# Performance work log

Measured on AMD Instinct MI355X. Metric: run time of the kernel, lower is better.

The kernel has to match this reference:

```python
import jax, jax.numpy as jnp
import numpy as np
from jax import lax

N_CLASS = 21
K_ED = 5
ALPHA = 0.1
BN_EPS = 1e-5


def _conv(x, w):
    # NCHW conv, stride 1, SAME padding
    return lax.conv_general_dilated(x, w, (1, 1), 'SAME',
                                    dimension_numbers=('NCHW', 'OIHW', 'NCHW'))


def _bn(x, g, b, m, v):
    # inference-mode BatchNorm2d with running stats
    scale = (g * lax.rsqrt(v + BN_EPS))[None, :, None, None]
    return (x - m[None, :, None, None]) * scale + b[None, :, None, None]


def _maxpool(x, k):
    return lax.reduce_window(x, -jnp.inf, lax.max, (1, 1, k, k), (1, 1, 1, 1), 'SAME')


def setup_inputs() -> dict:
    key = jax.random.key(0)
    ks = jax.random.split(key, 12)
    N, F, H, W, C = 8, 512, 96, 96, N_CLASS
    feature = jax.random.normal(ks[0], (N, F, H, W), jnp.float32)
    global_pred = jax.random.normal(ks[1], (N, C, H, W), jnp.float32)
    conv1_w = jax.random.normal(ks[2], (256, F, 3, 3), jnp.float32) * 0.02
    bn1_g = jnp.ones((256,), jnp.float32)
    bn1_b = jnp.zeros((256,), jnp.float32)
    bn1_m = jax.random.normal(ks[3], (256,), jnp.float32) * 0.1
    bn1_v = jax.random.uniform(ks[4], (256,), jnp.float32, 0.5, 1.5)
    conv2_w = jax.random.normal(ks[5], (128, 256, 3, 3), jnp.float32) * 0.02
    bn2_g = jnp.ones((128,), jnp.float32)
    bn2_b = jnp.zeros((128,), jnp.float32)
    bn2_m = jax.random.normal(ks[6], (128,), jnp.float32) * 0.1
    bn2_v = jax.random.uniform(ks[7], (128,), jnp.float32, 0.5, 1.5)
    conv3_w = jax.random.normal(ks[8], (C, 128, 1, 1), jnp.float32) * 0.02
    conv3_b = jnp.zeros((C,), jnp.float32)
    return dict(feature=feature, global_pred=global_pred,
                conv1_w=conv1_w, bn1_g=bn1_g, bn1_b=bn1_b, bn1_m=bn1_m, bn1_v=bn1_v,
                conv2_w=conv2_w, bn2_g=bn2_g, bn2_b=bn2_b, bn2_m=bn2_m, bn2_v=bn2_v,
                conv3_w=conv3_w, conv3_b=conv3_b)


def reference(feature, global_pred, conv1_w, bn1_g, bn1_b, bn1_m, bn1_v,
              conv2_w, bn2_g, bn2_b, bn2_m, bn2_v, conv3_w, conv3_b):
    N, F, H, W = feature.shape
    # hard labels -> one-hot [N, C, H, W]
    lbl = jnp.argmax(global_pred, axis=1)
    onehot = jnp.transpose(jax.nn.one_hot(lbl, N_CLASS, dtype=feature.dtype), (0, 3, 1, 2))
    # binary morphology: dilation = max-pool, erosion = -max-pool(-x)
    d = _maxpool(onehot, K_ED)
    e = -_maxpool(-onehot, K_ED)
    transition = jnp.sum(d - e, axis=1, keepdims=True)
    transition = jnp.where(transition >= 1.0, 1.0, transition)  # [N,1,H,W]
    tfeat = feature * transition
    # per-class masked mean over ALL H*W pixels (faithful to .mean(dim=2))
    objs = jnp.einsum('nfhw,nchw->ncf', feature, e) / (H * W)  # [N,C,F]
    # cdist(p=2) between transition-feature pixels and class prototypes
    x = tfeat.reshape(N, F, H * W).transpose(0, 2, 1)  # [N,HW,F]
    x2 = jnp.sum(x * x, axis=-1, keepdims=True)
    o2 = jnp.sum(objs * objs, axis=-1)
    d2 = jnp.maximum(x2 + o2[:, None, :] - 2.0 * jnp.einsum('npf,ncf->npc', x, objs), 0.0)
    cd = jnp.where(d2 > 0, jnp.sqrt(jnp.where(d2 > 0, d2, 1.0)), 0.0)  # safe sqrt
    dist = 1.0 - jax.nn.softmax(cd, axis=-1)  # [N,HW,C]
    obj_feat = jnp.einsum('npc,ncf->nfp', dist, objs).reshape(N, F, H, W)
    fusion = (feature * (1.0 - transition)
              + feature * transition * ALPHA
              + obj_feat * transition * (1.0 - ALPHA))
    # fusion_predictor: convBNReLU -> bilinear x2 -> convBNReLU -> 1x1 conv
    h = jax.nn.relu(_bn(_conv(fusion, conv1_w), bn1_g, bn1_b, bn1_m, bn1_v))
    h = jax.image.resize(h, (N, 256, 2 * H, 2 * W), method='bilinear')
    h = jax.nn.relu(_bn(_conv(h, conv2_w), bn2_g, bn2_b, bn2_m, bn2_v))
    logits = _conv(h, conv3_w) + conv3_b[None, :, None, None]
    # eval mode: softmax over classes
    return jax.nn.softmax(logits, axis=1)
```

## Files before the change

### kernel.cpp

```cpp
#include <hip/hip_runtime.h>
#include <cstdint>
#include <cstddef>

typedef __attribute__((ext_vector_type(4))) float f32x4;
typedef __attribute__((ext_vector_type(8))) short short8;

__device__ __forceinline__ float bf2f(unsigned short u) {
  union { unsigned int i; float f; } x; x.i = ((unsigned int)u) << 16; return x.f;
}
__device__ __forceinline__ unsigned short f2bf(float f) {
  union { float f; unsigned int i; } x; x.f = f;
  unsigned int r = x.i + 0x7fffu + ((x.i >> 16) & 1u);
  return (unsigned short)(r >> 16);
}
__device__ __forceinline__ void gload16(unsigned short* lds, const unsigned short* g) {
  __builtin_amdgcn_global_load_lds(
      (const __attribute__((address_space(1))) unsigned int*)g,
      (__attribute__((address_space(3))) unsigned int*)lds, 16, 0, 0);
}

__global__ void k_prep(const float* __restrict__ w1, const float* __restrict__ w2,
                       const float* __restrict__ w3,
                       const float* __restrict__ g1, const float* __restrict__ b1,
                       const float* __restrict__ m1, const float* __restrict__ v1,
                       const float* __restrict__ g2, const float* __restrict__ b2,
                       const float* __restrict__ m2, const float* __restrict__ v2,
                       unsigned short* __restrict__ w1t, unsigned short* __restrict__ w2t,
                       unsigned short* __restrict__ w3b,
                       float* __restrict__ s1, float* __restrict__ bb1,
                       float* __restrict__ s2, float* __restrict__ bb2) {
  const int blk = blockIdx.x;
  const int tid = threadIdx.x;
  if (blk < 4608) {
    int i = blk * 256 + tid;
    int o = i / 4608, k = i - o * 4608;
    int cblk = k / 288, r = k - cblk * 288;
    int t = r >> 5, cl = r & 31;
    int ci = cblk * 32 + cl;
    int ty = t / 3, tx = t - ty * 3;
    w1t[i] = f2bf(w1[((o * 512 + ci) * 3 + ty) * 3 + tx]);
  } else if (blk < 5760) {
    int i = (blk - 4608) * 256 + tid;
    int o = i / 2304, k = i - o * 2304;
    int cblk = k / 288, r = k - cblk * 288;
    int t = r >> 5, cl = r & 31;
    int ci = cblk * 32 + cl;
    int ty = t / 3, tx = t - ty * 3;
    w2t[i] = f2bf(w2[((o * 256 + ci) * 3 + ty) * 3 + tx]);
  } else if (blk < 5776) {
    int i = (blk - 5760) * 256 + tid;
    int c = i >> 7, k = i & 127;
    w3b[i] = (c < 21) ? f2bf(w3[c * 128 + k]) : (unsigned short)0;
  } else {
    if (tid < 256) { float s = g1[tid] * rsqrtf(v1[tid] + 1e-5f); s1[tid] = s; bb1[tid] = b1[tid] - m1[tid] * s; }
    if (tid < 128) { float s = g2[tid] * rsqrtf(v2[tid] + 1e-5f); s2[tid] = s; bb2[tid] = b2[tid] - m2[tid] * s; }
  }
}

__global__ void k_labels_init(const float* __restrict__ gp, signed char* __restrict__ lab,
                              unsigned short* __restrict__ fuP, float* __restrict__ objs) {
  const int blk = blockIdx.x;
  const int tid = threadIdx.x;
  if (blk < 288) {
    int p = blk * 256 + tid;
    int n = p / 9216, q = p - n * 9216;
    const float* g = gp + (long)n * 21 * 9216 + q;
    float best = g[0]; int bi = 0;
    #pragma unroll
    for (int c = 1; c < 21; c++) {
      float v = g[(long)c * 9216];
      if (v > best) { best = v; bi = c; }
    }
    lab[p] = (signed char)bi;
  } else if (blk < 1064) {
    int i = (blk - 288) * 256 + tid;
    const int B = 2 * 98 + 2 * 96;
    const int cg = i & 63; int b = i >> 6;
    const int n = b / B; b -= n * B;
    int y, x;
    if (b < 98) { y = 0; x = b; }
    else if (b < 196) { y = 97; x = b - 98; }
    else { int r = b - 196; y = 1 + (r >> 1); x = (r & 1) ? 97 : 0; }
    short8 z = {0, 0, 0, 0, 0, 0, 0, 0};
    *(short8*)&fuP[(((long)n * 98 + y) * 98 + x) * 512 + cg * 8] = z;
  } else {
    int i = (blk - 1064) * 256 + tid;
    objs[i] = 0.f;
  }
}

__global__ void k_em(const signed char* __restrict__ lab, signed char* __restrict__ em) {
  int p = blockIdx.x * 256 + threadIdx.x;
  int n = p / 9216, q = p - n * 9216, y = q / 96, x = q - y * 96;
  const signed char* L = lab + n * 9216;
  signed char l0 = L[q];
  bool uni = true;
  for (int dy = -2; dy <= 2; dy++) {
    int yy = y + dy; if (yy < 0 || yy > 95) continue;
    for (int dx = -2; dx <= 2; dx++) {
      int xx = x + dx; if (xx < 0 || xx > 95) continue;
      uni = uni && (L[yy * 96 + xx] == l0);
    }
  }
  em[p] = uni ? l0 : (signed char)-1;
}

__global__ __launch_bounds__(256)
void k_featT_objs(const float* __restrict__ feat, const signed char* __restrict__ em,
                  unsigned short* __restrict__ featT, float* __restrict__ objs) {
  __shared__ float part[21 * 128];
  __shared__ int pres[21];
  const int g = blockIdx.x * 256 + threadIdx.x;
  const int n = g / 9216, p = g - n * 9216;
  const int fg0 = blockIdx.y * 16;
  const int tid = threadIdx.x;
  for (int i = tid; i < 21 * 128; i += 256) part[i] = 0.f;
  if (tid < 21) pres[tid] = 0;
  __syncthreads();
  const int c0 = em[g];
  if (c0 >= 0) pres[c0] = 1;
  const float* src = feat + (long)n * 512 * 9216 + p;
  unsigned short* dst = featT + ((long)n * 9216 + p) * 512;
  for (int fg = fg0; fg < fg0 + 16; fg++) {
    short8 o;
    float fv[8];
    #pragma unroll
    for (int j = 0; j < 8; j++) {
      fv[j] = src[(long)(fg * 8 + j) * 9216];
      o[j] = (short)f2bf(fv[j]);
    }
    *(short8*)&dst[fg * 8] = o;
    if (c0 >= 0) {
      const int lf0 = (fg - fg0) * 8;
      #pragma unroll
      for (int j = 0; j < 8; j++) atomicAdd(&part[c0 * 128 + lf0 + j], fv[j]);
    }
  }
  __syncthreads();
  for (int i = tid; i < 21 * 128; i += 256) {
    const int c = i >> 7, lf = i & 127;
    if (pres[c])
      atomicAdd(&objs[((long)n * 21 + c) * 512 + blockIdx.y * 128 + lf],
                part[i] * (1.0f / 9216.0f));
  }
}

__global__ void k_objfin(const float* __restrict__ objs, float* __restrict__ o2,
                         unsigned short* __restrict__ oc) {
  const int b = blockIdx.x;
  const int n = b >> 5, c = b & 31;
  const int lane = threadIdx.x;
  unsigned short* dst = oc + ((long)n * 32 + c) * 512;
  if (c < 21) {
    const float* o = objs + ((long)n * 21 + c) * 512;
    float s = 0.f;
    for (int f = lane; f < 512; f += 64) {
      float v = o[f];
      s += v * v;
      dst[f] = f2bf(v);
    }
    #pragma unroll
    for (int off = 32; off; off >>= 1) s += __shfl_down(s, off);
    if (lane == 0) o2[n * 21 + c] = s;
  } else {
    for (int f = lane; f < 512; f += 64) dst[f] = 0;
  }
}

__global__ __launch_bounds__(256)
void k_dist_fusion(const unsigned short* __restrict__ featT,
                   const unsigned short* __restrict__ objs_c,
                   const float* __restrict__ o2, const float* __restrict__ objs,
                   const signed char* __restrict__ em,
                   unsigned short* __restrict__ fuP) {
  __shared__ float ob[21 * 512];
  __shared__ float dl[64][21];
  __shared__ signed char eml[64];
  const int n = blockIdx.y;
  const int p0 = blockIdx.x * 64;
  const int tid = threadIdx.x;
  const int w = tid >> 6, lane = tid & 63;
  const int lrow = lane & 15, kg = lane >> 4;

  for (int i = tid; i < 21 * 512; i += 256) ob[i] = objs[(long)n * 21 * 512 + i];
  if (tid < 64) eml[tid] = em[n * 9216 + p0 + tid];

  const int px = p0 + w * 16 + lrow;
  const unsigned short* fb = featT + ((long)n * 9216 + px) * 512 + kg * 8;
  const unsigned short* a0p = objs_c + ((long)n * 32 + lrow) * 512 + kg * 8;
  const unsigned short* a1p = a0p + 16 * 512;
  f32x4 acc0 = {0.f, 0.f, 0.f, 0.f}, acc1 = {0.f, 0.f, 0.f, 0.f};
  float x2 = 0.f;
  #pragma unroll
  for (int s = 0; s < 16; s++) {
    const short8 b = *(const short8*)&fb[s * 32];
    const short8 a0 = *(const short8*)&a0p[s * 32];
    const short8 a1 = *(const short8*)&a1p[s * 32];
    acc0 = __builtin_amdgcn_mfma_f32_16x16x32_bf16(a0, b, acc0, 0, 0, 0);
    acc1 = __builtin_amdgcn_mfma_f32_16x16x32_bf16(a1, b, acc1, 0, 0, 0);
    #pragma unroll
    for (int j = 0; j < 8; j++) { float v = bf2f((unsigned short)b[j]); x2 += v * v; }
  }
  x2 += __shfl_xor(x2, 16); x2 += __shfl_xor(x2, 32);
  float cd[8], mx = -1e30f;
  #pragma unroll
  for (int r = 0; r < 4; r++) {
    const int c = kg * 4 + r;
    float d2 = x2 + o2[n * 21 + c] - 2.f * acc0[r];
    cd[r] = sqrtf(fmaxf(d2, 0.f)); mx = fmaxf(mx, cd[r]);
  }
  #pragma unroll
  for (int r = 0; r < 4; r++) {
    const int c = 16 + kg * 4 + r;
    if (c < 21) {
      float d2 = x2 + o2[n * 21 + c] - 2.f * acc1[r];
      cd[4 + r] = sqrtf(fmaxf(d2, 0.f)); mx = fmaxf(mx, cd[4 + r]);
    } else cd[4 + r] = -1e30f;
  }
  mx = fmaxf(mx, __shfl_xor(mx, 16)); mx = fmaxf(mx, __shfl_xor(mx, 32));
  float sum = 0.f;
  #pragma unroll
  for (int k = 0; k < 8; k++) {
    cd[k] = (cd[k] > -1e29f) ? __expf(cd[k] - mx) : 0.f;
    sum += cd[k];
  }
  sum += __shfl_xor(sum, 16); sum += __shfl_xor(sum, 32);
  const float inv = 1.f / sum;
  const int lpx = w * 16 + lrow;
  #pragma unroll
  for (int r = 0; r < 4; r++) dl[lpx][kg * 4 + r] = 1.f - cd[r] * inv;
  #pragma unroll
  for (int r = 0; r < 4; r++) {
    const int c = 16 + kg * 4 + r;
    if (c < 21) dl[lpx][c] = 1.f - cd[4 + r] * inv;
  }
  __syncthreads();

  const int px2 = tid & 63;
  const int fg = (tid >> 6) * 8;
  const int q = p0 + px2;
  const int y = q / 96, x = q - y * 96;
  unsigned short* dst = fuP + (((long)n * 98 + y + 1) * 98 + (x + 1)) * 512;
  const bool t = eml[px2] < 0;
  const unsigned short* srcT = featT + ((long)n * 9216 + q) * 512;
  for (int f0 = 0; f0 < 512; f0 += 32) {
    short8 o;
    const short8 fvv = *(const short8*)&srcT[f0 + fg];
    #pragma unroll
    for (int j = 0; j < 8; j++) {
      const int f = f0 + fg + j;
      float fv = bf2f((unsigned short)fvv[j]);
      if (t) {
        float of = 0.f;
        #pragma unroll
        for (int c = 0; c < 21; c++) of += dl[px2][c] * ob[c * 512 + f];
        fv = 0.1f * fv + 0.9f * of;
      }
      o[j] = (short)f2bf(fv);
    }
    *(short8*)&dst[fg] = o;
    dst += 32;
  }
}

template <int CIN, int NK>
__global__ __launch_bounds__(256)
void conv3x3_gemm(const unsigned short* __restrict__ inP,
                  const unsigned short* __restrict__ wT,
                  const float* __restrict__ scale, const float* __restrict__ bias,
                  unsigned short* __restrict__ out,
                  int Hout, int Wout, int Hp, int Wp, int COUT, int nbN) {
  __shared__ unsigned short ldsA[3][4096];
  __shared__ unsigned short ldsB[3][4096];
  const int tid = threadIdx.x;
  const int chunk = gridDim.x >> 3;
  const int bid = (blockIdx.x & 7) * chunk + (blockIdx.x >> 3);
  const int mb = bid / nbN, nb = bid - mb * nbN;
  const int bm0 = mb * 128, bn0 = nb * 128;
  const int KT = 9 * CIN;
  const int HWo = Hout * Wout;

  const int rA = tid >> 2;
  const int ch8 = (((tid & 3) ^ ((tid >> 3) & 3)) * 8);
  const int m0 = bm0 + rA, m1 = m0 + 64;
  const int n0 = m0 / HWo; const int q0 = m0 - n0 * HWo;
  const int y0 = q0 / Wout, x0 = q0 - y0 * Wout;
  const int n1 = m1 / HWo; const int q1 = m1 - n1 * HWo;
  const int y1 = q1 / Wout, x1 = q1 - y1 * Wout;
  const unsigned short* gA0 = inP + ((long)(n0 * Hp + y0) * Wp + x0) * CIN + ch8;
  const unsigned short* gA1 = inP + ((long)(n1 * Hp + y1) * Wp + x1) * CIN + ch8;
  const unsigned short* gB0 = wT + (long)(bn0 + rA) * KT + ch8;
  const unsigned short* gB1 = wT + (long)(bn0 + rA + 64) * KT + ch8;

  const int lane = tid & 63;
  const int wv = tid >> 6;
  const int wr = wv >> 1, wc = wv & 1;
  const int lrow = lane & 15, kg = lane >> 4;
  const int arow = wr * 64 + lrow;
  const int aoff = arow * 32 + (kg ^ ((arow >> 1) & 3)) * 8;
  const int brow = wc * 64 + lrow;
  const int boff = brow * 32 + (kg ^ ((brow >> 1) & 3)) * 8;

  f32x4 acc[4][4];
  const f32x4 zero = {0.f, 0.f, 0.f, 0.f};
  #pragma unroll
  for (int i = 0; i < 4; i++)
    #pragma unroll
    for (int j = 0; j < 4; j++) acc[i][j] = zero;

  auto stage = [&](int b, int s) {
    const int cblk = s / 9;
    const int t = s - cblk * 9;
    const int ty = t / 3, tx = t - ty * 3;
    const long offA = (long)(ty * Wp + tx) * CIN + cblk * 32;
    gload16(&ldsA[b][tid * 8], gA0 + offA);
    gload16(&ldsA[b][2048 + tid * 8], gA1 + offA);
    const long k0 = (long)s * 32;
    gload16(&ldsB[b][tid * 8], gB0 + k0);
    gload16(&ldsB[b][2048 + tid * 8], gB1 + k0);
  };

  auto kstep = [&](int rd) {
    const unsigned short* A = ldsA[rd];
    const unsigned short* B = ldsB[rd];
    short8 af[4], bfr[4];
    #pragma unroll
    for (int i = 0; i < 4; i++) af[i] = *(const short8*)&A[aoff + i * 512];
    #pragma unroll
    for (int j = 0; j < 4; j++) bfr[j] = *(const short8*)&B[boff + j * 512];
    __builtin_amdgcn_s_setprio(1);
    #pragma unroll
    for (int i = 0; i < 4; i++)
      #pragma unroll
      for (int j = 0; j < 4; j++)
        acc[i][j] = __builtin_amdgcn_mfma_f32_16x16x32_bf16(af[i], bfr[j], acc[i][j], 0, 0, 0);
    __builtin_amdgcn_s_setprio(0);
  };

  stage(0, 0);
  stage(1, 1);
  int rd = 0, prev = 2;
  for (int s = 0; s < NK - 2; ++s) {
    __builtin_amdgcn_s_barrier();
    asm volatile("" ::: "memory");
    stage(prev, s + 2);
    asm volatile("s_waitcnt vmcnt(8)" ::: "memory");
    __builtin_amdgcn_s_barrier();
    asm volatile("" ::: "memory");
    kstep(rd);
    prev = rd; rd = (rd == 2) ? 0 : rd + 1;
  }
  asm volatile("s_waitcnt vmcnt(4)" ::: "memory");
  __builtin_amdgcn_s_barrier();
  asm volatile("" ::: "memory");
  kstep(rd);
  rd = (rd == 2) ? 0 : rd + 1;
  asm volatile("s_waitcnt vmcnt(0)" ::: "memory");
  __builtin_amdgcn_s_barrier();
  asm volatile("" ::: "memory");
  kstep(rd);

  #pragma unroll
  for (int i = 0; i < 4; i++) {
    const int row = bm0 + wr * 64 + i * 16 + kg * 4;
    #pragma unroll
    for (int j = 0; j < 4; j++) {
      const int col = bn0 + wc * 64 + j * 16 + lrow;
      const float sc = scale[col], bi = bias[col];
      #pragma unroll
      for (int r = 0; r < 4; r++) {
        float v = acc[i][j][r] * sc + bi;
        v = v > 0.f ? v : 0.f;
        out[(long)(row + r) * COUT + col] = f2bf(v);
      }
    }
  }
}

__global__ __launch_bounds__(256)
void conv2_fused(const unsigned short* __restrict__ inP,
                 const unsigned short* __restrict__ wT,
                 const float* __restrict__ scale, const float* __restrict__ bias,
                 const unsigned short* __restrict__ w3b, const float* __restrict__ b3,
                 float* __restrict__ out) {
  constexpr int CIN = 256, NK = 72;
  constexpr int Wout = 192, Hp = 194, Wp = 194;
  constexpr int HWo = 192 * 192;
  constexpr int KT = 9 * CIN;
  __shared__ unsigned short pool[6 * 4096];
  const int tid = threadIdx.x;
  const int chunk = gridDim.x >> 3;
  const int bid = (blockIdx.x & 7) * chunk + (blockIdx.x >> 3);
  const int bm0 = bid * 128;

  const int rA = tid >> 2;
  const int ch8 = (((tid & 3) ^ ((tid >> 3) & 3)) * 8);
  const int m0 = bm0 + rA, m1 = m0 + 64;
  const int n0 = m0 / HWo; const int q0 = m0 - n0 * HWo;
  const int y0 = q0 / Wout, x0 = q0 - y0 * Wout;
  const int n1 = m1 / HWo; const int q1 = m1 - n1 * HWo;
  const int y1 = q1 / Wout, x1 = q1 - y1 * Wout;
  const unsigned short* gA0 = inP + ((long)(n0 * Hp + y0) * Wp + x0) * CIN + ch8;
  const unsigned short* gA1 = inP + ((long)(n1 * Hp + y1) * Wp + x1) * CIN + ch8;
  const unsigned short* gB0 = wT + (long)rA * KT + ch8;
  const unsigned short* gB1 = wT + (long)(rA + 64) * KT + ch8;

  const int lane = tid & 63;
  const int wv = tid >> 6;
  const int wr = wv >> 1, wc = wv & 1;
  const int lrow = lane & 15, kg = lane >> 4;
  const int arow = wr * 64 + lrow;
  const int aoff = arow * 32 + (kg ^ ((arow >> 1) & 3)) * 8;
  const int brow = wc * 64 + lrow;
  const int boff = brow * 32 + (kg ^ ((brow >> 1) & 3)) * 8;

  f32x4 acc[4][4];
  const f32x4 zero = {0.f, 0.f, 0.f, 0.f};
  #pragma unroll
  for (int i = 0; i < 4; i++)
    #pragma unroll
    for (int j = 0; j < 4; j++) acc[i][j] = zero;

  auto stage = [&](int b, int s) {
    const int cblk = s / 9;
    const int t = s - cblk * 9;
    const int ty = t / 3, tx = t - ty * 3;
    const long offA = (long)(ty * Wp + tx) * CIN + cblk * 32;
    gload16(&pool[b * 4096 + tid * 8], gA0 + offA);
    gload16(&pool[b * 4096 + 2048 + tid * 8], gA1 + offA);
    const long k0 = (long)s * 32;
    gload16(&pool[12288 + b * 4096 + tid * 8], gB0 + k0);
    gload16(&pool[12288 + b * 4096 + 2048 + tid * 8], gB1 + k0);
  };

  auto kstep = [&](int rd) {
    const unsigned short* A = &pool[rd * 4096];
    const unsigned short* B = &pool[12288 + rd * 4096];
    short8 af[4], bfr[4];
    #pragma unroll
    for (int i = 0; i < 4; i++) af[i] = *(const short8*)&A[aoff + i * 512];
    #pragma unroll
    for (int j = 0; j < 4; j++) bfr[j] = *(const short8*)&B[boff + j * 512];
    __builtin_amdgcn_s_setprio(1);
    #pragma unroll
    for (int i = 0; i < 4; i++)
      #pragma unroll
      for (int j = 0; j < 4; j++)
        acc[i][j] = __builtin_amdgcn_mfma_f32_16x16x32_bf16(af[i], bfr[j], acc[i][j], 0, 0, 0);
    __builtin_amdgcn_s_setprio(0);
  };

  stage(0, 0);
  stage(1, 1);
  int rd = 0;
  for (int s = 0; s < NK; ++s) {
    if (s < NK - 1)
      asm volatile("s_waitcnt vmcnt(4)" ::: "memory");
    else
      asm volatile("s_waitcnt vmcnt(0)" ::: "memory");
    __builtin_amdgcn_s_barrier();
    asm volatile("" ::: "memory");
    kstep(rd);
    if (s + 2 < NK) stage((rd + 2 >= 3) ? rd - 1 : rd + 2, s + 2);
    rd = (rd == 2) ? 0 : rd + 1;
  }

  asm volatile("s_waitcnt lgkmcnt(0)" ::: "memory");
  __builtin_amdgcn_s_barrier();
  asm volatile("" ::: "memory");
  #pragma unroll
  for (int j = 0; j < 4; j++) {
    const int ch = wc * 64 + j * 16 + lrow;
    const float sc = scale[ch], bi = bias[ch];
    #pragma unroll
    for (int i = 0; i < 4; i++) {
      const int pxb = wr * 64 + i * 16 + kg * 4;
      #pragma unroll
      for (int r = 0; r < 4; r++) {
        const int px = pxb + r;
        float v = acc[i][j][r] * sc + bi;
        v = v > 0.f ? v : 0.f;
        pool[px * 128 + (ch ^ ((px & 7) << 3))] = f2bf(v);
      }
    }
  }
  asm volatile("s_waitcnt lgkmcnt(0)" ::: "memory");
  __builtin_amdgcn_s_barrier();
  asm volatile("" ::: "memory");

  #pragma unroll
  for (int g = 0; g < 2; g++) {
    const int px = wv * 32 + g * 16 + lrow;
    f32x4 acc0 = {0.f, 0.f, 0.f, 0.f}, acc1 = {0.f, 0.f, 0.f, 0.f};
    #pragma unroll
    for (int s = 0; s < 4; s++) {
      const int ch0 = s * 32 + kg * 8;
      const short8 b = *(const short8*)&pool[px * 128 + (ch0 ^ ((px & 7) << 3))];
      const short8 a0 = *(const short8*)&w3b[lrow * 128 + ch0];
      const short8 a1 = *(const short8*)&w3b[(16 + lrow) * 128 + ch0];
      acc0 = __builtin_amdgcn_mfma_f32_16x16x32_bf16(a0, b, acc0, 0, 0, 0);
      acc1 = __builtin_amdgcn_mfma_f32_16x16x32_bf16(a1, b, acc1, 0, 0, 0);
    }
    float lg[8], mx = -1e30f;
    #pragma unroll
    for (int r = 0; r < 4; r++) {
      lg[r] = acc0[r] + b3[kg * 4 + r];
      mx = fmaxf(mx, lg[r]);
    }
    #pragma unroll
    for (int r = 0; r < 4; r++) {
      const int c = 16 + kg * 4 + r;
      if (c < 21) { lg[4 + r] = acc1[r] + b3[c]; mx = fmaxf(mx, lg[4 + r]); }
      else lg[4 + r] = -1e30f;
    }
    mx = fmaxf(mx, __shfl_xor(mx, 16)); mx = fmaxf(mx, __shfl_xor(mx, 32));
    float sum = 0.f;
    #pragma unroll
    for (int k = 0; k < 8; k++) {
      lg[k] = (lg[k] > -1e29f) ? __expf(lg[k] - mx) : 0.f;
      sum += lg[k];
    }
    sum += __shfl_xor(sum, 16); sum += __shfl_xor(sum, 32);
    const float inv = 1.f / sum;
    const int m = bm0 + px;
    const int n = m / HWo;
    const int q = m - n * HWo;
    #pragma unroll
    for (int r = 0; r < 4; r++)
      out[((long)n * 21 + kg * 4 + r) * (long)HWo + q] = lg[r] * inv;
    #pragma unroll
    for (int r = 0; r < 4; r++) {
      const int c = 16 + kg * 4 + r;
      if (c < 21) out[((long)n * 21 + c) * (long)HWo + q] = lg[4 + r] * inv;
    }
  }
}

__global__ void k_upsample(const unsigned short* __restrict__ h1,
                           unsigned short* __restrict__ h2P) {
  if (blockIdx.x >= 36864) {
    int i = (blockIdx.x - 36864) * 256 + threadIdx.x;
    const int B = 2 * 194 + 2 * 192;
    const int cg = i & 31; int b = i >> 5;
    const int n = b / B; b -= n * B;
    int y, x;
    if (b < 194) { y = 0; x = b; }
    else if (b < 388) { y = 193; x = b - 194; }
    else { int r = b - 388; y = 1 + (r >> 1); x = (r & 1) ? 193 : 0; }
    short8 z = {0, 0, 0, 0, 0, 0, 0, 0};
    *(short8*)&h2P[(((long)n * 194 + y) * 194 + x) * 256 + cg * 8] = z;
    return;
  }
  const int idx = blockIdx.x * 256 + threadIdx.x;
  const int c8 = (idx & 31) * 8;
  const int p = idx >> 5;
  const int n = p / 36864; const int rr = p - n * 36864;
  const int Y = rr / 192, X = rr - Y * 192;
  const int ky = Y >> 1, kx = X >> 1;
  int yA, yB, xA, xB; float wyA, wyB, wxA, wxB;
  if ((Y & 1) == 0) { yA = ky > 0 ? ky - 1 : 0; yB = ky; wyA = 0.25f; wyB = 0.75f; }
  else { yA = ky; yB = ky < 95 ? ky + 1 : 95; wyA = 0.75f; wyB = 0.25f; }
  if ((X & 1) == 0) { xA = kx > 0 ? kx - 1 : 0; xB = kx; wxA = 0.25f; wxB = 0.75f; }
  else { xA = kx; xB = kx < 95 ? kx + 1 : 95; wxA = 0.75f; wxB = 0.25f; }
  const unsigned short* hb = h1 + (long)n * 96 * 96 * 256 + c8;
  const short8 vaa = *(const short8*)&hb[((long)yA * 96 + xA) * 256];
  const short8 vab = *(const short8*)&hb[((long)yA * 96 + xB) * 256];
  const short8 vba = *(const short8*)&hb[((long)yB * 96 + xA) * 256];
  const short8 vbb = *(const short8*)&hb[((long)yB * 96 + xB) * 256];
  short8 o;
  #pragma unroll
  for (int j = 0; j < 8; j++) {
    float v = wyA * (wxA * bf2f((unsigned short)vaa[j]) + wxB * bf2f((unsigned short)vab[j])) +
              wyB * (wxA * bf2f((unsigned short)vba[j]) + wxB * bf2f((unsigned short)vbb[j]));
    o[j] = (short)f2bf(v);
  }
  *(short8*)&h2P[(((long)n * 194 + Y + 1) * 194 + X + 1) * 256 + c8] = o;
}

extern "C" void kernel_launch(void* const* d_in, const int* in_sizes, int n_in,
                              void* d_out, int out_size, void* d_ws, size_t ws_size,
                              hipStream_t stream) {
  const float* feature = (const float*)d_in[0];
  const float* gp = (const float*)d_in[1];
  const float* w1 = (const float*)d_in[2];
  const float* g1 = (const float*)d_in[3];
  const float* b1 = (const float*)d_in[4];
  const float* m1 = (const float*)d_in[5];
  const float* v1 = (const float*)d_in[6];
  const float* w2 = (const float*)d_in[7];
  const float* g2 = (const float*)d_in[8];
  const float* b2 = (const float*)d_in[9];
  const float* m2 = (const float*)d_in[10];
  const float* v2 = (const float*)d_in[11];
  const float* w3 = (const float*)d_in[12];
  const float* b3 = (const float*)d_in[13];
  float* out = (float*)d_out;

  char* ws = (char*)d_ws;
  size_t off = 0;
  auto alloc = [&](size_t bytes) -> void* {
    void* p = ws + off;
    off += (bytes + 255) & ~(size_t)255;
    return p;
  };
  signed char* lab = (signed char*)alloc(73728);
  signed char* em = (signed char*)alloc(73728);
  float* objs = (float*)alloc(8 * 21 * 512 * 4);
  float* o2 = (float*)alloc(168 * 4);
  unsigned short* objs_c = (unsigned short*)alloc((size_t)8 * 32 * 512 * 2);
  unsigned short* w1t = (unsigned short*)alloc((size_t)256 * 4608 * 2);
  unsigned short* w2t = (unsigned short*)alloc((size_t)128 * 2304 * 2);
  unsigned short* w3b = (unsigned short*)alloc((size_t)32 * 128 * 2);
  float* s1 = (float*)alloc(256 * 4);
  float* bb1 = (float*)alloc(256 * 4);
  float* s2 = (float*)alloc(128 * 4);
  float* bb2 = (float*)alloc(128 * 4);
  const size_t fuP_bytes = (size_t)8 * 98 * 98 * 512 * 2;
  unsigned short* fuP = (unsigned short*)alloc(fuP_bytes);
  const size_t h1_bytes = (size_t)8 * 96 * 96 * 256 * 2;
  unsigned short* h1 = (unsigned short*)alloc(h1_bytes);
  const size_t h2P_bytes = (size_t)8 * 194 * 194 * 256 * 2;
  unsigned short* h2P = (unsigned short*)alloc(h2P_bytes);
  unsigned short* featT = h2P;

  if (off > ws_size) return;

  k_prep<<<5777, 256, 0, stream>>>(w1, w2, w3, g1, b1, m1, v1, g2, b2, m2, v2,
                                   w1t, w2t, w3b, s1, bb1, s2, bb2);
  k_labels_init<<<1400, 256, 0, stream>>>(gp, lab, fuP, objs);
  k_em<<<288, 256, 0, stream>>>(lab, em);
  k_featT_objs<<<dim3(288, 4), 256, 0, stream>>>(feature, em, featT, objs);
  k_objfin<<<256, 64, 0, stream>>>(objs, o2, objs_c);
  k_dist_fusion<<<dim3(144, 8), 256, 0, stream>>>(featT, objs_c, o2, objs, em, fuP);

  conv3x3_gemm<512, 144><<<1152, 256, 0, stream>>>(fuP, w1t, s1, bb1, h1,
                                                   96, 96, 98, 98, 256, 2);
  k_upsample<<<37636, 256, 0, stream>>>(h1, h2P);
  conv2_fused<<<2304, 256, 0, stream>>>(h2P, w2t, s2, bb2, w3b, b3, out);
}
```

Before: 720.8 us.

## Widen conv1 GEMM tile to cover all 256 output channels per block

```diff
diff --git a/kernel.cpp b/kernel.cpp
--- a/kernel.cpp
+++ b/kernel.cpp
@@ -263,22 +263,21 @@
   }
 }
 
-template <int CIN, int NK>
-__global__ __launch_bounds__(256)
-void conv3x3_gemm(const unsigned short* __restrict__ inP,
-                  const unsigned short* __restrict__ wT,
-                  const float* __restrict__ scale, const float* __restrict__ bias,
-                  unsigned short* __restrict__ out,
-                  int Hout, int Wout, int Hp, int Wp, int COUT, int nbN) {
-  __shared__ unsigned short ldsA[3][4096];
-  __shared__ unsigned short ldsB[3][4096];
+__global__ __launch_bounds__(256, 2)
+void conv1_wide(const unsigned short* __restrict__ inP,
+                const unsigned short* __restrict__ wT,
+                const float* __restrict__ scale, const float* __restrict__ bias,
+                unsigned short* __restrict__ out) {
+  constexpr int CIN = 512, NK = 144;
+  constexpr int Wout = 96, Hp = 98, Wp = 98;
+  constexpr int HWo = 96 * 96;
+  constexpr int KT = 9 * CIN;
+  __shared__ unsigned short ldsA[2][4096];
+  __shared__ unsigned short ldsB[2][8192];
   const int tid = threadIdx.x;
   const int chunk = gridDim.x >> 3;
   const int bid = (blockIdx.x & 7) * chunk + (blockIdx.x >> 3);
-  const int mb = bid / nbN, nb = bid - mb * nbN;
-  const int bm0 = mb * 128, bn0 = nb * 128;
-  const int KT = 9 * CIN;
-  const int HWo = Hout * Wout;
+  const int bm0 = bid * 128;
 
   const int rA = tid >> 2;
   const int ch8 = (((tid & 3) ^ ((tid >> 3) & 3)) * 8);
@@ -289,22 +288,21 @@
   const int y1 = q1 / Wout, x1 = q1 - y1 * Wout;
   const unsigned short* gA0 = inP + ((long)(n0 * Hp + y0) * Wp + x0) * CIN + ch8;
   const unsigned short* gA1 = inP + ((long)(n1 * Hp + y1) * Wp + x1) * CIN + ch8;
-  const unsigned short* gB0 = wT + (long)(bn0 + rA) * KT + ch8;
-  const unsigned short* gB1 = wT + (long)(bn0 + rA + 64) * KT + ch8;
+  const unsigned short* gB[4];
+  #pragma unroll
+  for (int k = 0; k < 4; k++) gB[k] = wT + (long)(rA + 64 * k) * KT + ch8;
 
   const int lane = tid & 63;
   const int wv = tid >> 6;
-  const int wr = wv >> 1, wc = wv & 1;
   const int lrow = lane & 15, kg = lane >> 4;
-  const int arow = wr * 64 + lrow;
-  const int aoff = arow * 32 + (kg ^ ((arow >> 1) & 3)) * 8;
-  const int brow = wc * 64 + lrow;
-  const int boff = brow * 32 + (kg ^ ((brow >> 1) & 3)) * 8;
-
-  f32x4 acc[4][4];
+  const int aoff = lrow * 32 + ((kg ^ ((lrow >> 1) & 3)) * 8);
+  const int brow0 = wv * 64 + lrow;
+  const int boff = brow0 * 32 + ((kg ^ ((brow0 >> 1) & 3)) * 8);
+
+  f32x4 acc[8][4];
   const f32x4 zero = {0.f, 0.f, 0.f, 0.f};
   #pragma unroll
-  for (int i = 0; i < 4; i++)
+  for (int i = 0; i < 8; i++)
     #pragma unroll
     for (int j = 0; j < 4; j++) acc[i][j] = zero;
 
@@ -316,21 +314,22 @@
     gload16(&ldsA[b][tid * 8], gA0 + offA);
     gload16(&ldsA[b][2048 + tid * 8], gA1 + offA);
     const long k0 = (long)s * 32;
-    gload16(&ldsB[b][tid * 8], gB0 + k0);
-    gload16(&ldsB[b][2048 + tid * 8], gB1 + k0);
+    #pragma unroll
+    for (int k = 0; k < 4; k++)
+      gload16(&ldsB[b][k * 2048 + tid * 8], gB[k] + k0);
   };
 
   auto kstep = [&](int rd) {
     const unsigned short* A = ldsA[rd];
     const unsigned short* B = ldsB[rd];
-    short8 af[4], bfr[4];
-    #pragma unroll
-    for (int i = 0; i < 4; i++) af[i] = *(const short8*)&A[aoff + i * 512];
+    short8 af[8], bfr[4];
+    #pragma unroll
+    for (int i = 0; i < 8; i++) af[i] = *(const short8*)&A[aoff + i * 512];
     #pragma unroll
     for (int j = 0; j < 4; j++) bfr[j] = *(const short8*)&B[boff + j * 512];
     __builtin_amdgcn_s_setprio(1);
     #pragma unroll
-    for (int i = 0; i < 4; i++)
+    for (int i = 0; i < 8; i++)
       #pragma unroll
       for (int j = 0; j < 4; j++)
         acc[i][j] = __builtin_amdgcn_mfma_f32_16x16x32_bf16(af[i], bfr[j], acc[i][j], 0, 0, 0);
@@ -339,39 +338,31 @@
 
   stage(0, 0);
   stage(1, 1);
-  int rd = 0, prev = 2;
-  for (int s = 0; s < NK - 2; ++s) {
+  for (int s = 0; s < NK; ++s) {
+    if (s < NK - 1)
+      asm volatile("s_waitcnt vmcnt(6)" ::: "memory");
+    else
+      asm volatile("s_waitcnt vmcnt(0)" ::: "memory");
     __builtin_amdgcn_s_barrier();
     asm volatile("" ::: "memory");
-    stage(prev, s + 2);
-    asm volatile("s_waitcnt vmcnt(8)" ::: "memory");
+    kstep(s & 1);
     __builtin_amdgcn_s_barrier();
     asm volatile("" ::: "memory");
-    kstep(rd);
-    prev = rd; rd = (rd == 2) ? 0 : rd + 1;
-  }
-  asm volatile("s_waitcnt vmcnt(4)" ::: "memory");
-  __builtin_amdgcn_s_barrier();
-  asm volatile("" ::: "memory");
-  kstep(rd);
-  rd = (rd == 2) ? 0 : rd + 1;
-  asm volatile("s_waitcnt vmcnt(0)" ::: "memory");
-  __builtin_amdgcn_s_barrier();
-  asm volatile("" ::: "memory");
-  kstep(rd);
-
-  #pragma unroll
-  for (int i = 0; i < 4; i++) {
-    const int row = bm0 + wr * 64 + i * 16 + kg * 4;
+    if (s + 2 < NK) stage(s & 1, s + 2);
+  }
+
+  #pragma unroll
+  for (int i = 0; i < 8; i++) {
+    const int row = bm0 + i * 16 + kg * 4;
     #pragma unroll
     for (int j = 0; j < 4; j++) {
-      const int col = bn0 + wc * 64 + j * 16 + lrow;
+      const int col = wv * 64 + j * 16 + lrow;
       const float sc = scale[col], bi = bias[col];
       #pragma unroll
       for (int r = 0; r < 4; r++) {
         float v = acc[i][j][r] * sc + bi;
         v = v > 0.f ? v : 0.f;
-        out[(long)(row + r) * COUT + col] = f2bf(v);
+        out[(long)(row + r) * 256 + col] = f2bf(v);
       }
     }
   }
@@ -633,8 +624,7 @@
   k_objfin<<<256, 64, 0, stream>>>(objs, o2, objs_c);
   k_dist_fusion<<<dim3(144, 8), 256, 0, stream>>>(featT, objs_c, o2, objs, em, fuP);
 
-  conv3x3_gemm<512, 144><<<1152, 256, 0, stream>>>(fuP, w1t, s1, bb1, h1,
-                                                   96, 96, 98, 98, 256, 2);
+  conv1_wide<<<576, 256, 0, stream>>>(fuP, w1t, s1, bb1, h1);
   k_upsample<<<37636, 256, 0, stream>>>(h1, h2P);
   conv2_fused<<<2304, 256, 0, stream>>>(h2P, w2t, s2, bb2, w3b, b3, out);
 }
```

Result: slower. 761.9 us (+5.7%).
